# Optimization experiments

Measured on AMD Instinct MI355X. Metric: run time of the kernel, lower is better.

Reference implementation:

```python
import jax, jax.numpy as jnp
import numpy as np

LORA_SCALING = 16.0 / 8.0  # lora_alpha / lora_r


def setup_inputs() -> dict:
    key = jax.random.key(0)
    k_x, k_m, k_wm, k_bm, k_wa, k_wb = jax.random.split(key, 6)
    B, S, D_in, D_out, R = 4, 2048, 4096, 4096, 8
    x = jax.random.normal(k_x, (B, S, D_in), dtype=jnp.float32)
    im_mask = jax.random.randint(k_m, (B, S), 0, 2) > 0  # bool token mask
    # Linear weights stored torch-style: [out, in]
    W_main = jax.random.normal(k_wm, (D_out, D_in), dtype=jnp.float32) * (1.0 / np.sqrt(D_in))
    b_main = jax.random.normal(k_bm, (D_out,), dtype=jnp.float32) * 0.01
    W_A = jax.random.normal(k_wa, (R, D_in), dtype=jnp.float32) * (1.0 / np.sqrt(D_in))
    W_B = jax.random.normal(k_wb, (D_out, R), dtype=jnp.float32) * (1.0 / np.sqrt(R))
    return {"x": x, "im_mask": im_mask, "W_main": W_main, "b_main": b_main, "W_A": W_A, "W_B": W_B}


def reference(x, im_mask, W_main, b_main, W_A, W_B):
    # Main dense path: res = x @ W_main.T + b
    res = jnp.einsum('bsd,od->bso', x, W_main) + b_main
    # LoRA path applied only at masked tokens (dropout disabled / eval):
    # res[im_mask] += (x[im_mask] @ W_A.T) @ W_B.T * scaling
    # Static-shape equivalent: compute everywhere, mask the add.
    lora = jnp.einsum('bsr,or->bso', jnp.einsum('bsd,rd->bsr', x, W_A), W_B)
    return res + jnp.where(im_mask[..., None], lora * LORA_SCALING, jnp.zeros((), x.dtype))
```

## Files before the change

kernel.cpp:

```cpp
#include <hip/hip_runtime.h>

typedef unsigned short u16;
typedef unsigned int   u32;
typedef unsigned long long u64;
typedef __bf16 bf16x8 __attribute__((ext_vector_type(8)));
typedef float  f32x4  __attribute__((ext_vector_type(4)));

#define AS1 __attribute__((address_space(1)))
#define AS3 __attribute__((address_space(3)))

#define M_TOK 8192
#define K_DIM 4096
#define N_DIM 4096
#define BK    32
#define NKT   (K_DIM / BK)

static __device__ __forceinline__ u16 f2bf(float f) {
  u32 u = __builtin_bit_cast(u32, f);
  return (u16)((u + (0x7FFFu + ((u >> 16) & 1u))) >> 16);
}

static __device__ __forceinline__ void gld_lds16(const void* g, void* l) {
  __builtin_amdgcn_global_load_lds((AS1 u32*)(u64)g, (AS3 u32*)(u32)(u64)l, 16, 0, 0);
}

__global__ __launch_bounds__(256) void k_conv_w(const float* __restrict__ W,
                                                u16* __restrict__ Wb, int n4) {
  const float4* W4 = (const float4*)W;
  ushort4* Wb4 = (ushort4*)Wb;
  int i = blockIdx.x * 256 + threadIdx.x;
  const int stride = gridDim.x * 256;
  for (; i < n4; i += stride) {
    float4 v = W4[i];
    ushort4 o;
    o.x = f2bf(v.x); o.y = f2bf(v.y); o.z = f2bf(v.z); o.w = f2bf(v.w);
    Wb4[i] = o;
  }
}

__global__ __launch_bounds__(256) void k_prep_x(const float* __restrict__ x,
                                                const float* __restrict__ WA,
                                                u16* __restrict__ xb,
                                                float* __restrict__ mid) {
  const int m = blockIdx.x;
  const int t = threadIdx.x;
  const float4* xr = (const float4*)(x + (size_t)m * K_DIM);
  ushort4* xbr = (ushort4*)(xb + (size_t)m * K_DIM);
  float a[8] = {0.f,0.f,0.f,0.f,0.f,0.f,0.f,0.f};
  #pragma unroll
  for (int i = 0; i < 4; ++i) {
    const int k4 = t + i * 256;
    float4 v = xr[k4];
    ushort4 o;
    o.x = f2bf(v.x); o.y = f2bf(v.y); o.z = f2bf(v.z); o.w = f2bf(v.w);
    xbr[k4] = o;
    #pragma unroll
    for (int r = 0; r < 8; ++r) {
      float4 wv = ((const float4*)(WA + (size_t)r * K_DIM))[k4];
      a[r] += v.x * wv.x + v.y * wv.y + v.z * wv.z + v.w * wv.w;
    }
  }
  #pragma unroll
  for (int r = 0; r < 8; ++r) {
    #pragma unroll
    for (int off = 32; off > 0; off >>= 1)
      a[r] += __shfl_down(a[r], off);
  }
  __shared__ float red[4][8];
  const int w = t >> 6, l = t & 63;
  if (l == 0) {
    #pragma unroll
    for (int r = 0; r < 8; ++r) red[w][r] = a[r];
  }
  __syncthreads();
  if (t < 8)
    mid[(size_t)m * 8 + t] = 2.0f * (red[0][t] + red[1][t] + red[2][t] + red[3][t]);
}

__global__ __launch_bounds__(512, 2) void k_gemm(
    const u16* __restrict__ A, const u16* __restrict__ B,
    const float* __restrict__ bias, const int* __restrict__ mask,
    const float* __restrict__ mid, const float* __restrict__ WBw,
    float* __restrict__ out) {
  __shared__ u16 smem[4][2][256][BK];

  const int t = threadIdx.x;
  const int wid = t >> 6, l = t & 63;
  const int wr = wid >> 2, wc = wid & 3;
  const int fr = l & 15, fq = l >> 4;

  const int bid = blockIdx.x;
  const int swz = (bid & 7) * 64 + (bid >> 3);
  const int bm = swz >> 4, bn = swz & 15;

  const char* Ag = (const char*)(A + (size_t)bm * 256 * K_DIM);
  const char* Bg = (const char*)(B + (size_t)bn * 256 * K_DIM);
  const size_t rowb = (size_t)K_DIM * 2;

  const int srow = t >> 2;
  const int schk = (((t & 3) ^ ((t >> 3) & 3)) * 16);
  const char* bA0 = Ag + (size_t)srow * rowb + schk;
  const char* bA1 = Ag + (size_t)(128 + srow) * rowb + schk;
  const char* bB0 = Bg + (size_t)srow * rowb + schk;
  const char* bB1 = Bg + (size_t)(128 + srow) * rowb + schk;
  char* lbase = (char*)&smem[0][0][0][0] + wid * 1024;

  f32x4 acc[8][4];
  #pragma unroll
  for (int m = 0; m < 8; ++m)
    #pragma unroll
    for (int n = 0; n < 4; ++n)
      acc[m][n] = (f32x4){0.f, 0.f, 0.f, 0.f};

  #pragma unroll
  for (int pk = 0; pk < 3; ++pk) {
    gld_lds16(bA0 + pk * 64, lbase + pk * 32768);
    gld_lds16(bA1 + pk * 64, lbase + pk * 32768 + 8192);
    gld_lds16(bB0 + pk * 64, lbase + pk * 32768 + 16384);
    gld_lds16(bB1 + pk * 64, lbase + pk * 32768 + 24576);
  }
  asm volatile("s_waitcnt vmcnt(8)");
  __builtin_amdgcn_s_barrier();

  const int csw = (fq ^ ((fr >> 1) & 3)) * 8;

  const char* gA0 = bA0 + 192;
  const char* gA1 = bA1 + 192;
  const char* gB0 = bB0 + 192;
  const char* gB1 = bB1 + 192;

  #define K_TILE(BUFC, NB, DOSTAGE, GOFF, WAIT) do {                         \
    const u16* Ab_ = &smem[BUFC][0][wr * 128 + fr][csw];                     \
    const u16* Bb_ = &smem[BUFC][1][wc * 64 + fr][csw];                      \
    bf16x8 af_[4], bf_[4];                                                   \
    _Pragma("unroll")                                                        \
    for (int m = 0; m < 4; ++m) af_[m] = *(const bf16x8*)(Ab_ + m * 16 * BK);\
    _Pragma("unroll")                                                        \
    for (int n = 0; n < 4; ++n) bf_[n] = *(const bf16x8*)(Bb_ + n * 16 * BK);\
    if (DOSTAGE) {                                                           \
      gld_lds16(gA0 + (GOFF), lbase + (NB) * 32768);                         \
      gld_lds16(gA1 + (GOFF), lbase + (NB) * 32768 + 8192);                  \
    }                                                                        \
    __builtin_amdgcn_s_barrier();                                            \
    asm volatile("s_waitcnt lgkmcnt(0)");                                    \
    __builtin_amdgcn_s_setprio(1);                                           \
    _Pragma("unroll")                                                        \
    for (int m = 0; m < 4; ++m)                                              \
      _Pragma("unroll")                                                      \
      for (int n = 0; n < 4; ++n)                                            \
        acc[m][n] = __builtin_amdgcn_mfma_f32_16x16x32_bf16(                 \
            af_[m], bf_[n], acc[m][n], 0, 0, 0);                             \
    __builtin_amdgcn_s_setprio(0);                                           \
    __builtin_amdgcn_s_barrier();                                            \
    _Pragma("unroll")                                                        \
    for (int m = 0; m < 4; ++m)                                              \
      af_[m] = *(const bf16x8*)(Ab_ + (4 + m) * 16 * BK);                    \
    if (DOSTAGE) {                                                           \
      gld_lds16(gB0 + (GOFF), lbase + (NB) * 32768 + 16384);                 \
      gld_lds16(gB1 + (GOFF), lbase + (NB) * 32768 + 24576);                 \
    }                                                                        \
    WAIT;                                                                    \
    __builtin_amdgcn_s_barrier();                                            \
    asm volatile("s_waitcnt lgkmcnt(0)");                                    \
    __builtin_amdgcn_s_setprio(1);                                           \
    _Pragma("unroll")                                                        \
    for (int m = 0; m < 4; ++m)                                              \
      _Pragma("unroll")                                                      \
      for (int n = 0; n < 4; ++n)                                            \
        acc[4 + m][n] = __builtin_amdgcn_mfma_f32_16x16x32_bf16(             \
            af_[m], bf_[n], acc[4 + m][n], 0, 0, 0);                         \
    __builtin_amdgcn_s_setprio(0);                                           \
    __builtin_amdgcn_s_barrier();                                            \
  } while (0)

  #define VM8 asm volatile("s_waitcnt vmcnt(8)")
  #define VM4 asm volatile("s_waitcnt vmcnt(4)")
  #define VM0 asm volatile("s_waitcnt vmcnt(0)")

  for (int ktb = 0; ktb < NKT - 4; ktb += 4) {
    K_TILE(0, 3, true, 0,   VM8);
    K_TILE(1, 0, true, 64,  VM8);
    K_TILE(2, 1, true, 128, VM8);
    K_TILE(3, 2, true, 192, VM8);
    gA0 += 256; gA1 += 256; gB0 += 256; gB1 += 256;
  }
  K_TILE(0, 3, true,  0, VM8);
  K_TILE(1, 0, false, 0, VM4);
  K_TILE(2, 1, false, 0, VM0);
  K_TILE(3, 2, false, 0, ((void)0));

  #undef K_TILE
  #undef VM8
  #undef VM4
  #undef VM0

  const int gn0 = bn * 256 + wc * 64;
  const size_t gm0 = (size_t)bm * 256 + wr * 128;
  float wbv[4][8]; float bv[4];
  #pragma unroll
  for (int n = 0; n < 4; ++n) {
    const int gn = gn0 + n * 16 + fr;
    bv[n] = bias[gn];
    const float4 w0 = ((const float4*)(WBw + (size_t)gn * 8))[0];
    const float4 w1 = ((const float4*)(WBw + (size_t)gn * 8))[1];
    wbv[n][0] = w0.x; wbv[n][1] = w0.y; wbv[n][2] = w0.z; wbv[n][3] = w0.w;
    wbv[n][4] = w1.x; wbv[n][5] = w1.y; wbv[n][6] = w1.z; wbv[n][7] = w1.w;
  }
  #pragma unroll
  for (int m = 0; m < 8; ++m) {
    #pragma unroll
    for (int j = 0; j < 4; ++j) {
      const size_t gm = gm0 + m * 16 + fq * 4 + j;
      const int msk = mask[gm];
      const float4 m0 = ((const float4*)(mid + gm * 8))[0];
      const float4 m1 = ((const float4*)(mid + gm * 8))[1];
      float* orow = out + gm * (size_t)N_DIM;
      #pragma unroll
      for (int n = 0; n < 4; ++n) {
        const float lora =
            m0.x * wbv[n][0] + m0.y * wbv[n][1] + m0.z * wbv[n][2] + m0.w * wbv[n][3] +
            m1.x * wbv[n][4] + m1.y * wbv[n][5] + m1.z * wbv[n][6] + m1.w * wbv[n][7];
        orow[gn0 + n * 16 + fr] = acc[m][n][j] + bv[n] + (msk ? lora : 0.0f);
      }
    }
  }
}

extern "C" void kernel_launch(void* const* d_in, const int* in_sizes, int n_in,
                              void* d_out, int out_size, void* d_ws, size_t ws_size,
                              hipStream_t stream) {
  (void)in_sizes; (void)n_in; (void)out_size; (void)ws_size;
  const float* x     = (const float*)d_in[0];
  const int*   mask  = (const int*)d_in[1];
  const float* Wm    = (const float*)d_in[2];
  const float* bmain = (const float*)d_in[3];
  const float* WA    = (const float*)d_in[4];
  const float* WB    = (const float*)d_in[5];
  float* out = (float*)d_out;

  u16* xb  = (u16*)d_ws;
  u16* wb  = xb + (size_t)M_TOK * K_DIM;
  float* mid = (float*)(wb + (size_t)N_DIM * K_DIM);

  k_conv_w<<<2048, 256, 0, stream>>>(Wm, wb, (N_DIM * K_DIM) / 4);
  k_prep_x<<<M_TOK, 256, 0, stream>>>(x, WA, xb, mid);
  dim3 grid((M_TOK / 256) * (N_DIM / 256));
  k_gemm<<<grid, 512, 0, stream>>>(xb, wb, bmain, mask, mid, WB, out);
}
```

Baseline: 336.6 us.

## Collapse GEMM K-tile into a single phase and merge the prep kernels

The GEMM inner K-tile no longer splits into two half-phases separated by several barriers. It now reads all eight A fragments and four B fragments up front, issues all four global-to-LDS stage loads at once, runs the full 8x4 MFMA block, and ends with a single barrier. This removes three workgroup barriers and an explicit lgkmcnt wait per K step, at the cost of more live VGPRs and less interleaving between LDS reads and MFMAs. The weight-conversion and x-prep kernels are also merged into one launch, with extra blocks handling the bf16 conversion of the weights, which saves a kernel launch and lets both jobs run concurrently.

New measurement: 325.9 us. 3.2% less time.

```diff
diff --git a/kernel.cpp b/kernel.cpp
--- a/kernel.cpp
+++ b/kernel.cpp
@@ -24,26 +24,28 @@
   __builtin_amdgcn_global_load_lds((AS1 u32*)(u64)g, (AS3 u32*)(u32)(u64)l, 16, 0, 0);
 }
 
-__global__ __launch_bounds__(256) void k_conv_w(const float* __restrict__ W,
-                                                u16* __restrict__ Wb, int n4) {
-  const float4* W4 = (const float4*)W;
-  ushort4* Wb4 = (ushort4*)Wb;
-  int i = blockIdx.x * 256 + threadIdx.x;
-  const int stride = gridDim.x * 256;
-  for (; i < n4; i += stride) {
-    float4 v = W4[i];
-    ushort4 o;
-    o.x = f2bf(v.x); o.y = f2bf(v.y); o.z = f2bf(v.z); o.w = f2bf(v.w);
-    Wb4[i] = o;
-  }
-}
-
-__global__ __launch_bounds__(256) void k_prep_x(const float* __restrict__ x,
-                                                const float* __restrict__ WA,
-                                                u16* __restrict__ xb,
-                                                float* __restrict__ mid) {
+__global__ __launch_bounds__(256) void k_prep(const float* __restrict__ x,
+                                              const float* __restrict__ WA,
+                                              const float* __restrict__ W,
+                                              u16* __restrict__ xb,
+                                              float* __restrict__ mid,
+                                              u16* __restrict__ Wb) {
+  const int t = threadIdx.x;
+  if (blockIdx.x >= M_TOK) {
+    const int cb = blockIdx.x - M_TOK;
+    const float4* W4 = (const float4*)W;
+    ushort4* Wb4 = (ushort4*)Wb;
+    const int n4 = (N_DIM * K_DIM) / 4;
+    int i = cb * 256 + t;
+    for (; i < n4; i += 2048 * 256) {
+      float4 v = W4[i];
+      ushort4 o;
+      o.x = f2bf(v.x); o.y = f2bf(v.y); o.z = f2bf(v.z); o.w = f2bf(v.w);
+      Wb4[i] = o;
+    }
+    return;
+  }
   const int m = blockIdx.x;
-  const int t = threadIdx.x;
   const float4* xr = (const float4*)(x + (size_t)m * K_DIM);
   ushort4* xbr = (ushort4*)(xb + (size_t)m * K_DIM);
   float a[8] = {0.f,0.f,0.f,0.f,0.f,0.f,0.f,0.f};
@@ -132,44 +134,26 @@
   #define K_TILE(BUFC, NB, DOSTAGE, GOFF, WAIT) do {                         \
     const u16* Ab_ = &smem[BUFC][0][wr * 128 + fr][csw];                     \
     const u16* Bb_ = &smem[BUFC][1][wc * 64 + fr][csw];                      \
-    bf16x8 af_[4], bf_[4];                                                   \
+    bf16x8 af_[8], bf_[4];                                                   \
     _Pragma("unroll")                                                        \
-    for (int m = 0; m < 4; ++m) af_[m] = *(const bf16x8*)(Ab_ + m * 16 * BK);\
+    for (int m = 0; m < 8; ++m) af_[m] = *(const bf16x8*)(Ab_ + m * 16 * BK);\
     _Pragma("unroll")                                                        \
     for (int n = 0; n < 4; ++n) bf_[n] = *(const bf16x8*)(Bb_ + n * 16 * BK);\
     if (DOSTAGE) {                                                           \
       gld_lds16(gA0 + (GOFF), lbase + (NB) * 32768);                         \
       gld_lds16(gA1 + (GOFF), lbase + (NB) * 32768 + 8192);                  \
+      gld_lds16(gB0 + (GOFF), lbase + (NB) * 32768 + 16384);                 \
+      gld_lds16(gB1 + (GOFF), lbase + (NB) * 32768 + 24576);                 \
     }                                                                        \
-    __builtin_amdgcn_s_barrier();                                            \
-    asm volatile("s_waitcnt lgkmcnt(0)");                                    \
     __builtin_amdgcn_s_setprio(1);                                           \
     _Pragma("unroll")                                                        \
-    for (int m = 0; m < 4; ++m)                                              \
+    for (int m = 0; m < 8; ++m)                                              \
       _Pragma("unroll")                                                      \
       for (int n = 0; n < 4; ++n)                                            \
         acc[m][n] = __builtin_amdgcn_mfma_f32_16x16x32_bf16(                 \
             af_[m], bf_[n], acc[m][n], 0, 0, 0);                             \
     __builtin_amdgcn_s_setprio(0);                                           \
-    __builtin_amdgcn_s_barrier();                                            \
-    _Pragma("unroll")                                                        \
-    for (int m = 0; m < 4; ++m)                                              \
-      af_[m] = *(const bf16x8*)(Ab_ + (4 + m) * 16 * BK);                    \
-    if (DOSTAGE) {                                                           \
-      gld_lds16(gB0 + (GOFF), lbase + (NB) * 32768 + 16384);                 \
-      gld_lds16(gB1 + (GOFF), lbase + (NB) * 32768 + 24576);                 \
-    }                                                                        \
     WAIT;                                                                    \
-    __builtin_amdgcn_s_barrier();                                            \
-    asm volatile("s_waitcnt lgkmcnt(0)");                                    \
-    __builtin_amdgcn_s_setprio(1);                                           \
-    _Pragma("unroll")                                                        \
-    for (int m = 0; m < 4; ++m)                                              \
-      _Pragma("unroll")                                                      \
-      for (int n = 0; n < 4; ++n)                                            \
-        acc[4 + m][n] = __builtin_amdgcn_mfma_f32_16x16x32_bf16(             \
-            af_[m], bf_[n], acc[4 + m][n], 0, 0, 0);                         \
-    __builtin_amdgcn_s_setprio(0);                                           \
     __builtin_amdgcn_s_barrier();                                            \
   } while (0)
 
@@ -242,8 +226,7 @@
   u16* wb  = xb + (size_t)M_TOK * K_DIM;
   float* mid = (float*)(wb + (size_t)N_DIM * K_DIM);
 
-  k_conv_w<<<2048, 256, 0, stream>>>(Wm, wb, (N_DIM * K_DIM) / 4);
-  k_prep_x<<<M_TOK, 256, 0, stream>>>(x, WA, xb, mid);
+  k_prep<<<M_TOK + 2048, 256, 0, stream>>>(x, WA, Wm, xb, mid, wb);
   dim3 grid((M_TOK / 256) * (N_DIM / 256));
   k_gemm<<<grid, 512, 0, stream>>>(xb, wb, bmain, mask, mid, WB, out);
 }
```
